# Kernel optimization log

Measured on AMD Instinct MI355X. Metric: run time of the kernel, lower is better.

## Reference

```python
import jax, jax.numpy as jnp
import numpy as np

DIM = 768   # embedding dim
NH = 12     # num heads
HD = DIM // NH  # head dim = 64
WS = 14     # window size
EPS = 1e-5  # nn.LayerNorm default


def _ln(x, w, b):
    m = jnp.mean(x, -1, keepdims=True)
    v = jnp.var(x, -1, keepdims=True)
    return (x - m) * jax.lax.rsqrt(v + EPS) * w + b


def setup_inputs() -> dict:
    key = jax.random.key(0)
    ks = jax.random.split(key, 8)
    def n(k, shape, s=0.02):
        return jax.random.normal(k, shape, jnp.float32) * s
    return {
        "x": jax.random.normal(ks[0], (4, 64, 64, DIM), jnp.float32),
        "ln1_w": jnp.ones((DIM,), jnp.float32),
        "ln1_b": jnp.zeros((DIM,), jnp.float32),
        "qkv_w": n(ks[1], (DIM, 3 * DIM)),
        "qkv_b": jnp.zeros((3 * DIM,), jnp.float32),
        "proj_w": n(ks[2], (DIM, DIM)),
        "proj_b": jnp.zeros((DIM,), jnp.float32),
        "rel_pos_h": n(ks[3], (2 * WS - 1, HD)),
        "rel_pos_w": n(ks[4], (2 * WS - 1, HD)),
        "ln2_w": jnp.ones((DIM,), jnp.float32),
        "ln2_b": jnp.zeros((DIM,), jnp.float32),
        "fc1_w": n(ks[5], (DIM, 4 * DIM)),
        "fc1_b": jnp.zeros((4 * DIM,), jnp.float32),
        "fc2_w": n(ks[6], (4 * DIM, DIM)),
        "fc2_b": jnp.zeros((DIM,), jnp.float32),
    }


def _block(x, ln1_w, ln1_b, qkv_w, qkv_b, proj_w, proj_b,
           rel_pos_h, rel_pos_w, ln2_w, ln2_b, fc1_w, fc1_b, fc2_w, fc2_b):
    B, H, W, C = x.shape
    shortcut = x
    xn = _ln(x, ln1_w, ln1_b)

    # ---- window partition (pad H,W up to multiples of WS) ----
    pad_h = (-H) % WS
    pad_w = (-W) % WS
    xp = jnp.pad(xn, ((0, 0), (0, pad_h), (0, pad_w), (0, 0)))
    Hp, Wp = H + pad_h, W + pad_w
    nh, nw = Hp // WS, Wp // WS
    xw = xp.reshape(B, nh, WS, nw, WS, C).transpose(0, 1, 3, 2, 4, 5)
    xw = xw.reshape(B * nh * nw, WS, WS, C)  # [Bw, ws, ws, C]
    Bw = B * nh * nw
    N = WS * WS

    # ---- attention with decomposed relative position bias ----
    qkv = xw.reshape(Bw, N, C) @ qkv_w + qkv_b            # [Bw, N, 3C]
    qkv = qkv.reshape(Bw, N, 3, NH, HD).transpose(2, 0, 3, 1, 4)  # [3, Bw, NH, N, HD]
    q, k, v = qkv[0], qkv[1], qkv[2]
    scale = HD ** -0.5
    attn = jnp.einsum("bhnd,bhmd->bhnm", q * scale, k)    # [Bw, NH, N, N]

    # decomposed rel pos: Rh[q_h, k_h, c], Rw[q_w, k_w, c]
    idx = jnp.arange(WS)[:, None] - jnp.arange(WS)[None, :] + (WS - 1)
    Rh = rel_pos_h[idx]  # [ws, ws, HD]
    Rw = rel_pos_w[idx]  # [ws, ws, HD]
    rq = q.reshape(Bw, NH, WS, WS, HD)
    rel_h = jnp.einsum("bnhwc,hkc->bnhwk", rq, Rh)  # over q rows vs k rows
    rel_w = jnp.einsum("bnhwc,wkc->bnhwk", rq, Rw)  # over q cols vs k cols
    attn = (attn.reshape(Bw, NH, WS, WS, WS, WS)
            + rel_h[..., :, None] + rel_w[..., None, :]).reshape(Bw, NH, N, N)

    attn = jax.nn.softmax(attn, axis=-1)
    out = jnp.einsum("bhnm,bhmd->bhnd", attn, v)          # [Bw, NH, N, HD]
    out = out.transpose(0, 2, 1, 3).reshape(Bw, WS, WS, C)
    out = out @ proj_w + proj_b

    # ---- window unpartition + crop padding ----
    out = out.reshape(B, nh, nw, WS, WS, C).transpose(0, 1, 3, 2, 4, 5)
    out = out.reshape(B, Hp, Wp, C)[:, :H, :W, :]

    x = shortcut + out

    # ---- MLP ----
    h = _ln(x, ln2_w, ln2_b)
    h = jax.nn.gelu(h @ fc1_w + fc1_b, approximate=False)
    x = x + (h @ fc2_w + fc2_b)
    return x


def reference(x, ln1_w, ln1_b, qkv_w, qkv_b, proj_w, proj_b,
              rel_pos_h, rel_pos_w, ln2_w, ln2_b, fc1_w, fc1_b, fc2_w, fc2_b):
    return _block(x, ln1_w, ln1_b, qkv_w, qkv_b, proj_w, proj_b,
                  rel_pos_h, rel_pos_w, ln2_w, ln2_b, fc1_w, fc1_b, fc2_w, fc2_b)
```

## Files before the change

### kernel.cpp

```cpp
#include <hip/hip_runtime.h>

typedef unsigned short u16;
typedef __bf16 bf16x8_t __attribute__((ext_vector_type(8)));
typedef float f32x4_t __attribute__((ext_vector_type(4)));

__device__ __forceinline__ float bf2f(u16 u) {
    union { unsigned u; float f; } c; c.u = ((unsigned)u) << 16; return c.f;
}
__device__ __forceinline__ u16 f2bf(float f) {
    union { float f; unsigned u; } c; c.f = f;
    unsigned u = c.u;
    unsigned r = (u + 0x7FFFu + ((u >> 16) & 1u)) >> 16;
    return (u16)r;
}

__device__ __forceinline__ void gld16(const u16* g, u16* l) {
    __builtin_amdgcn_global_load_lds(
        (const __attribute__((address_space(1))) unsigned*)g,
        (__attribute__((address_space(3))) unsigned*)l, 16, 0, 0);
}

__device__ __forceinline__ void block_sum2(float& s, float& sq) {
    for (int o = 32; o > 0; o >>= 1) { s += __shfl_xor(s, o); sq += __shfl_xor(sq, o); }
    __shared__ float sh[8];
    int wid = threadIdx.x >> 6;
    if ((threadIdx.x & 63) == 0) { sh[wid] = s; sh[4 + wid] = sq; }
    __syncthreads();
    s  = sh[0] + sh[1] + sh[2] + sh[3];
    sq = sh[4] + sh[5] + sh[6] + sh[7];
}

__global__ __launch_bounds__(256) void ln1_window(
    const float* __restrict__ x, const float* __restrict__ w, const float* __restrict__ b,
    u16* __restrict__ out, int row0)
{
    int lrow = blockIdx.x, tid = threadIdx.x;
    int wr = row0 + lrow;
    int wb = wr / 196, t = wr % 196;
    int gh = ((wb % 25) / 5) * 14 + t / 14;
    int gw = (wb % 5) * 14 + t % 14;
    size_t orow = (size_t)lrow * 768;
    __shared__ u16 rowbuf[768];
    if (gh >= 64 || gw >= 64) {
        rowbuf[tid] = 0; rowbuf[tid + 256] = 0; rowbuf[tid + 512] = 0;
        __syncthreads();
        if (tid < 96) *(uint4*)&out[orow + (tid << 3)] = *(const uint4*)&rowbuf[tid << 3];
        return;
    }
    size_t base = (size_t)(((wb / 25) * 64 + gh) * 64 + gw) * 768;
    float v0 = x[base + tid], v1 = x[base + tid + 256], v2 = x[base + tid + 512];
    float s = v0 + v1 + v2, sq = v0 * v0 + v1 * v1 + v2 * v2;
    block_sum2(s, sq);
    float mean = s * (1.0f / 768.0f);
    float var  = sq * (1.0f / 768.0f) - mean * mean;
    float inv  = rsqrtf(var + 1e-5f);
    rowbuf[tid]       = f2bf((v0 - mean) * inv * w[tid]       + b[tid]);
    rowbuf[tid + 256] = f2bf((v1 - mean) * inv * w[tid + 256] + b[tid + 256]);
    rowbuf[tid + 512] = f2bf((v2 - mean) * inv * w[tid + 512] + b[tid + 512]);
    __syncthreads();
    if (tid < 96) *(uint4*)&out[orow + (tid << 3)] = *(const uint4*)&rowbuf[tid << 3];
}

__global__ __launch_bounds__(256) void ln2_chunk(
    const float* __restrict__ xin, const float* __restrict__ w, const float* __restrict__ b,
    u16* __restrict__ out)
{
    int row = blockIdx.x, tid = threadIdx.x;
    size_t base = (size_t)row * 768;
    __shared__ u16 rowbuf[768];
    float v0 = xin[base + tid], v1 = xin[base + tid + 256], v2 = xin[base + tid + 512];
    float s = v0 + v1 + v2, sq = v0 * v0 + v1 * v1 + v2 * v2;
    block_sum2(s, sq);
    float mean = s * (1.0f / 768.0f);
    float var  = sq * (1.0f / 768.0f) - mean * mean;
    float inv  = rsqrtf(var + 1e-5f);
    rowbuf[tid]       = f2bf((v0 - mean) * inv * w[tid]       + b[tid]);
    rowbuf[tid + 256] = f2bf((v1 - mean) * inv * w[tid + 256] + b[tid + 256]);
    rowbuf[tid + 512] = f2bf((v2 - mean) * inv * w[tid + 512] + b[tid + 512]);
    __syncthreads();
    if (tid < 96) *(uint4*)&out[base + (tid << 3)] = *(const uint4*)&rowbuf[tid << 3];
}

__global__ __launch_bounds__(256) void transpose_wf(
    const float* __restrict__ in, u16* __restrict__ out, int K, int N)
{
    __shared__ u16 t[32][33];
    __shared__ u16 tt[32][32];
    int n0 = blockIdx.x * 32, k0 = blockIdx.y * 32;
    int tx = threadIdx.x & 31, ty = threadIdx.x >> 5;
    for (int q = 0; q < 4; q++) {
        int k = k0 + ty + q * 8, n = n0 + tx;
        t[ty + q * 8][tx] = (k < K && n < N) ? f2bf(in[(size_t)k * N + n]) : (u16)0;
    }
    __syncthreads();
    for (int q = 0; q < 4; q++) tt[ty + q * 8][tx] = t[tx][ty + q * 8];
    __syncthreads();
    if (threadIdx.x < 128) {
        int r = threadIdx.x >> 2, c8 = (threadIdx.x & 3) << 3;
        int n = n0 + r, k = k0 + c8;
        if (n < N && k < K)
            *(uint4*)&out[(size_t)n * K + k] = *(const uint4*)&tt[r][c8];
    }
}

__global__ __launch_bounds__(256) void build_relT(
    const float* __restrict__ rh, const float* __restrict__ rw, u16* __restrict__ out)
{
    int i = blockIdx.x * 256 + threadIdx.x;
    int r = i >> 6, c = i & 63;
    float v = (r < 27) ? rh[r * 64 + c] : (r < 54 ? rw[(r - 27) * 64 + c] : 0.f);
    out[i] = f2bf(v);
}

__global__ __launch_bounds__(256) void build_vt(
    const u16* __restrict__ qkvc, u16* __restrict__ vt)
{
    int z = blockIdx.x;
    int wb = z / 12, h = z % 12;
    __shared__ u16 t[64][232];
    int tid = threadIdx.x;
    for (int base = 0; base < 196; base += 4) {
        int m = base + (tid >> 6);
        int d = tid & 63;
        t[d][m] = qkvc[(size_t)(wb * 196 + m) * 2304 + 1536 + h * 64 + d];
    }
    for (int idx = tid; idx < 28 * 64; idx += 256) {
        int m = 196 + idx / 64, d = idx % 64;
        t[d][m] = 0;
    }
    __syncthreads();
    size_t ob = (size_t)z * 64 * 224;
    for (int idx = tid; idx < 64 * 28; idx += 256) {
        int d = idx / 28, c8 = (idx % 28) << 3;
        *(uint4*)&vt[ob + (size_t)d * 224 + c8] = *(const uint4*)&t[d][c8];
    }
}

__global__ __launch_bounds__(256) void softmax_rel2(
    u16* __restrict__ S, const u16* __restrict__ G2)
{
    int z = blockIdx.y;
    int wv = threadIdx.x >> 6, lane = threadIdx.x & 63;
    int n = blockIdx.x * 4 + wv;
    size_t srow = (size_t)z * 196 * 224 + (size_t)n * 224;
    const u16* g2 = G2 + (size_t)z * 196 * 64 + (size_t)n * 64;
    int qh = n / 14, qw = n % 14;
    float s[4];
    for (int c = 0; c < 4; c++) {
        int m = c * 64 + lane;
        if (m < 196) {
            int kk = m / 14, jj = m % 14;
            float bh = bf2f(g2[qh - kk + 13]);
            float bw = bf2f(g2[27 + qw - jj + 13]);
            s[c] = 0.125f * bf2f(S[srow + m]) + bh + bw;
        } else s[c] = -1e30f;
    }
    float mx = fmaxf(fmaxf(s[0], s[1]), fmaxf(s[2], s[3]));
    for (int o = 32; o > 0; o >>= 1) mx = fmaxf(mx, __shfl_xor(mx, o));
    float e[4], sm = 0.f;
    for (int c = 0; c < 4; c++) {
        int m = c * 64 + lane;
        e[c] = (m < 196) ? expf(s[c] - mx) : 0.f;
        sm += e[c];
    }
    for (int o = 32; o > 0; o >>= 1) sm += __shfl_xor(sm, o);
    float inv = 1.0f / sm;
    for (int c = 0; c < 4; c++) {
        int m = c * 64 + lane;
        if (m < 224) S[srow + m] = f2bf(e[c] * inv);
    }
}

__device__ __forceinline__ int swz_off(int row, int kcElem) {
    return row * 32 + (kcElem ^ (((row >> 1) & 3) << 3));
}

template <int MODE>
__global__ __launch_bounds__(256, 3) void gemm_nt(
    const u16* __restrict__ Aall, const u16* __restrict__ Ball,
    const float* __restrict__ bias, const float* xf,
    u16* __restrict__ Cb, float* Cf, int M, int row0)
{
    constexpr int BK = 32;
    int N, K, lda, ldb;
    size_t aoff = 0, boff = 0, coff = 0;
    if constexpr (MODE == 0) { N = 2304; K = 768; lda = 768; ldb = 768; }
    else if constexpr (MODE == 1) {
        N = 196; K = 64; lda = 2304; ldb = 2304;
        int z = blockIdx.z;
        aoff = (size_t)(z / 12) * 196 * 2304 + (size_t)(z % 12) * 64;
        boff = aoff + 768;
        coff = (size_t)z * 196 * 224;
    } else if constexpr (MODE == 2) {
        N = 64; K = 224; lda = 224; ldb = 224;
        int z = blockIdx.z;
        aoff = (size_t)z * 196 * 224;
        boff = (size_t)z * 64 * 224;
        coff = (size_t)(z / 12) * 196 * 768 + (size_t)(z % 12) * 64;
    } else if constexpr (MODE == 3) { N = 768; K = 768; lda = 768; ldb = 768; }
    else if constexpr (MODE == 4) { N = 3072; K = 768; lda = 768; ldb = 768; }
    else if constexpr (MODE == 6) {
        N = 64; K = 64; lda = 2304; ldb = 64;
        int z = blockIdx.z;
        aoff = (size_t)(z / 12) * 196 * 2304 + (size_t)(z % 12) * 64;
        boff = 0;
        coff = (size_t)z * 196 * 64;
    }
    else { N = 768; K = 3072; lda = 3072; ldb = 3072; }

    __shared__ __align__(16) u16 smem[24576];

    int tid = threadIdx.x, wid = tid >> 6, lane = tid & 63;
    int quad = lane >> 4, l16 = lane & 15;

    int bx = blockIdx.x, by = blockIdx.y;
    if constexpr (MODE != 1 && MODE != 2 && MODE != 6) {
        int gX = gridDim.x;
        int nwg = gX * gridDim.y;
        int orig = by * gX + bx;
        int q = nwg >> 3, r = nwg & 7;
        int xcd = orig & 7, idx = orig >> 3;
        int wg = (xcd < r ? xcd * (q + 1) : r * (q + 1) + (xcd - r) * q) + idx;
        bx = wg % gX; by = wg / gX;
    }
    int m_tile = by * 128, n_tile = bx * 128;
    int wm0 = (wid >> 1) * 64, wn0 = (wid & 1) * 64;

    const u16* A = Aall + aoff;
    const u16* B = Ball + boff;

    const u16* gA[2]; const u16* gB[2];
    int loff[2];
    {
        int s = lane & 3, rofs = lane >> 2;
        for (int j = 0; j < 2; j++) {
            int r0 = wid * 32 + j * 16;
            int rr = r0 + rofs;
            int xr = (rr >> 1) & 3;
            int colo = ((s ^ xr) << 3);
            int am = m_tile + rr; if (am > M - 1) am = M - 1;
            int bn = n_tile + rr; if (bn > N - 1) bn = N - 1;
            gA[j] = A + (size_t)am * lda + colo;
            gB[j] = B + (size_t)bn * ldb + colo;
            loff[j] = r0 * 32;
        }
    }

    f32x4_t acc[4][4];
    f32x4_t z4 = {0.f, 0.f, 0.f, 0.f};
    for (int mt = 0; mt < 4; mt++)
        for (int nt = 0; nt < 4; nt++) acc[mt][nt] = z4;

    int nsteps = K / BK;
    for (int j = 0; j < 2; j++) {
        gld16(gA[j], smem + loff[j]);
        gld16(gB[j], smem + 4096 + loff[j]);
    }
    for (int j = 0; j < 2; j++) {
        gld16(gA[j] + BK, smem + 8192 + loff[j]);
        gld16(gB[j] + BK, smem + 12288 + loff[j]);
    }

    int cur = 0;
    for (int k = 0; k < nsteps; k++) {
        if (k + 1 < nsteps) {
            asm volatile("s_waitcnt vmcnt(4)" ::: "memory");
        } else {
            asm volatile("s_waitcnt vmcnt(0)" ::: "memory");
        }
        __builtin_amdgcn_sched_barrier(0);
        __builtin_amdgcn_s_barrier();
        __builtin_amdgcn_sched_barrier(0);
        if (k + 2 < nsteps) {
            int nb = cur + 2; if (nb >= 3) nb -= 3;
            u16* dst = smem + nb * 8192;
            int kn = (k + 2) * BK;
            for (int j = 0; j < 2; j++) {
                gld16(gA[j] + kn, dst + loff[j]);
                gld16(gB[j] + kn, dst + 4096 + loff[j]);
            }
        }
        const u16* Ac = smem + cur * 8192;
        const u16* Bc = Ac + 4096;
        bf16x8_t af[4], bfv[4];
        for (int t = 0; t < 4; t++) {
            int ar = wm0 + t * 16 + l16;
            int br = wn0 + t * 16 + l16;
            af[t]  = *(const bf16x8_t*)&Ac[swz_off(ar, quad * 8)];
            bfv[t] = *(const bf16x8_t*)&Bc[swz_off(br, quad * 8)];
        }
        for (int mt = 0; mt < 4; mt++)
            for (int nt = 0; nt < 4; nt++)
                acc[mt][nt] = __builtin_amdgcn_mfma_f32_16x16x32_bf16(
                    af[mt], bfv[nt], acc[mt][nt], 0, 0, 0);
        cur++; if (cur >= 3) cur -= 3;
    }

    if constexpr (MODE == 0 || MODE == 1 || MODE == 2 || MODE == 4 || MODE == 6) {
        u16* Cs = smem;
        int ldc = (MODE == 0) ? 2304 : (MODE == 1) ? 224 : (MODE == 2) ? 768
                : (MODE == 6) ? 64 : 3072;
        int colmax = (MODE == 1) ? 224 : N;
        for (int half = 0; half < 2; half++) {
            __syncthreads();
            if ((wm0 >> 6) == half) {
                for (int mt = 0; mt < 4; mt++) {
                    int rl = mt * 16 + quad * 4;
                    for (int nt = 0; nt < 4; nt++) {
                        int cl = wn0 + nt * 16 + l16;
                        int col = n_tile + cl;
                        for (int rg = 0; rg < 4; rg++) {
                            float v = acc[mt][nt][rg];
                            u16 o;
                            if constexpr (MODE == 0) o = f2bf(v + bias[col]);
                            else if constexpr (MODE == 4) {
                                float g = v + bias[col];
                                o = f2bf(0.5f * g * (1.0f + erff(g * 0.70710678118f)));
                            } else o = f2bf(v);
                            Cs[(rl + rg) * 136 + cl] = o;
                        }
                    }
                }
            }
            __syncthreads();
            for (int it = 0; it < 4; it++) {
                int chunk = tid + it * 256;
                int r = chunk >> 4, c8 = (chunk & 15) << 3;
                int grow = m_tile + half * 64 + r, gcol = n_tile + c8;
                if (grow >= M || gcol >= colmax) continue;
                *(uint4*)&Cb[coff + (size_t)grow * ldc + gcol] =
                    *(const uint4*)&Cs[r * 136 + c8];
            }
        }
    } else {
        float* Cfs = (float*)smem;
        for (int q = 0; q < 4; q++) {
            __syncthreads();
            if ((wm0 >> 6) == (q >> 1)) {
                for (int mt2 = 0; mt2 < 2; mt2++) {
                    int mt = (q & 1) * 2 + mt2;
                    int rloc = mt2 * 16 + quad * 4;
                    for (int nt = 0; nt < 4; nt++) {
                        int cl = wn0 + nt * 16 + l16;
                        for (int rg = 0; rg < 4; rg++)
                            Cfs[(rloc + rg) * 132 + cl] = acc[mt][nt][rg];
                    }
                }
            }
            __syncthreads();
            for (int it = 0; it < 4; it++) {
                int chunk = tid + it * 256;
                int r = chunk >> 5, c4 = (chunk & 31) << 2;
                int grow = m_tile + q * 32 + r;
                int gcol = n_tile + c4;
                if (grow >= M || gcol >= N) continue;
                f32x4_t v4 = *(const f32x4_t*)&Cfs[r * 132 + c4];
                f32x4_t b4 = *(const f32x4_t*)&bias[gcol];
                if constexpr (MODE == 5) {
                    size_t idx = (size_t)(row0 + grow) * 768 + gcol;
                    f32x4_t x4 = *(const f32x4_t*)&xf[idx];
                    f32x4_t o4;
                    for (int j = 0; j < 4; j++) o4[j] = v4[j] + x4[j] + b4[j];
                    *(f32x4_t*)&Cf[idx] = o4;
                } else {
                    int wr = row0 + grow;
                    int wb2 = wr / 196, t2 = wr % 196;
                    int gh = ((wb2 % 25) / 5) * 14 + t2 / 14;
                    int gw = (wb2 % 5) * 14 + t2 % 14;
                    if (gh < 64 && gw < 64) {
                        size_t g = (size_t)(((wb2 / 25) * 64 + gh) * 64 + gw) * 768 + gcol;
                        f32x4_t x4 = *(const f32x4_t*)&xf[g];
                        f32x4_t o4;
                        for (int j = 0; j < 4; j++) o4[j] = v4[j] + x4[j] + b4[j];
                        *(f32x4_t*)&Cf[g] = o4;
                    }
                }
            }
        }
    }
}

extern "C" void kernel_launch(void* const* d_in, const int* in_sizes, int n_in,
                              void* d_out, int out_size, void* d_ws, size_t ws_size,
                              hipStream_t stream)
{
    (void)in_sizes; (void)n_in; (void)out_size;
    const float* x      = (const float*)d_in[0];
    const float* ln1_w  = (const float*)d_in[1];
    const float* ln1_b  = (const float*)d_in[2];
    const float* qkv_w  = (const float*)d_in[3];
    const float* qkv_b  = (const float*)d_in[4];
    const float* proj_w = (const float*)d_in[5];
    const float* proj_b = (const float*)d_in[6];
    const float* rel_h  = (const float*)d_in[7];
    const float* rel_w  = (const float*)d_in[8];
    const float* ln2_w  = (const float*)d_in[9];
    const float* ln2_b  = (const float*)d_in[10];
    const float* fc1_w  = (const float*)d_in[11];
    const float* fc1_b  = (const float*)d_in[12];
    const float* fc2_w  = (const float*)d_in[13];
    const float* fc2_b  = (const float*)d_in[14];

    const size_t WT = 14155776ull + 8192ull;
    char* ws = (char*)d_ws;
    u16* qkvT  = (u16*)ws;
    u16* projT = qkvT + 2304 * 768;
    u16* fc1T  = projT + 768 * 768;
    u16* fc2T  = fc1T + 3072 * 768;
    u16* relT  = fc2T + 3072 * 768;
    char* scratch = ws + WT;
    size_t avail = (ws_size > WT) ? (ws_size - WT) : 0;

    const size_t perW = 3204096ull;
    static const int wc_cand[8] = {100, 50, 25, 20, 10, 5, 2, 1};
    int Wc = 1;
    for (int i = 0; i < 8; i++) {
        if ((size_t)wc_cand[i] * perW <= avail) { Wc = wc_cand[i]; break; }
    }
    static const int rm_cand[8] = {16384, 8192, 4096, 2048, 1024, 512, 256, 128};
    int Rm = 128;
    for (int i = 0; i < 8; i++) {
        if ((size_t)rm_cand[i] * 7680ull <= avail) { Rm = rm_cand[i]; break; }
    }

    u16* lnwc  = (u16*)scratch;
    u16* qkvc  = (u16*)(scratch + (size_t)Wc * 301056ull);
    u16* Sc    = (u16*)(scratch + (size_t)Wc * 1204224ull);
    u16* vtc   = (u16*)(scratch + (size_t)Wc * 2257920ull);
    u16* attnc = (u16*)(scratch + (size_t)Wc * 2601984ull);
    u16* G2c   = (u16*)(scratch + (size_t)Wc * 2903040ull);
    u16* hbuf  = (u16*)scratch;
    u16* xn2c  = (u16*)(scratch + (size_t)Rm * 6144ull);
    float* dout = (float*)d_out;

    transpose_wf<<<dim3(72, 24), 256, 0, stream>>>(qkv_w, qkvT, 768, 2304);
    transpose_wf<<<dim3(24, 24), 256, 0, stream>>>(proj_w, projT, 768, 768);
    transpose_wf<<<dim3(96, 24), 256, 0, stream>>>(fc1_w, fc1T, 768, 3072);
    transpose_wf<<<dim3(24, 96), 256, 0, stream>>>(fc2_w, fc2T, 3072, 768);
    build_relT<<<16, 256, 0, stream>>>(rel_h, rel_w, relT);

    int nch = 100 / Wc;
    int rows = Wc * 196;
    int gy = (rows + 127) / 128;
    for (int c = 0; c < nch; c++) {
        int r0 = c * rows;
        ln1_window<<<rows, 256, 0, stream>>>(x, ln1_w, ln1_b, lnwc, r0);
        gemm_nt<0><<<dim3(18, gy), 256, 0, stream>>>(
            lnwc, qkvT, qkv_b, nullptr, qkvc, nullptr, rows, 0);
        gemm_nt<1><<<dim3(2, 2, Wc * 12), 256, 0, stream>>>(
            qkvc, qkvc, nullptr, nullptr, Sc, nullptr, 196, 0);
        gemm_nt<6><<<dim3(1, 2, Wc * 12), 256, 0, stream>>>(
            qkvc, relT, nullptr, nullptr, G2c, nullptr, 196, 0);
        build_vt<<<Wc * 12, 256, 0, stream>>>(qkvc, vtc);
        softmax_rel2<<<dim3(49, Wc * 12), 256, 0, stream>>>(Sc, G2c);
        gemm_nt<2><<<dim3(1, 2, Wc * 12), 256, 0, stream>>>(
            Sc, vtc, nullptr, nullptr, attnc, nullptr, 196, 0);
        gemm_nt<3><<<dim3(6, gy), 256, 0, stream>>>(
            attnc, projT, proj_b, x, nullptr, dout, rows, r0);
    }

    int nm = 16384 / Rm;
    for (int c = 0; c < nm; c++) {
        int r0 = c * Rm;
        ln2_chunk<<<Rm, 256, 0, stream>>>(dout + (size_t)r0 * 768, ln2_w, ln2_b, xn2c);
        gemm_nt<4><<<dim3(24, Rm / 128), 256, 0, stream>>>(
            xn2c, fc1T, fc1_b, nullptr, hbuf, nullptr, Rm, 0);
        gemm_nt<5><<<dim3(6, Rm / 128), 256, 0, stream>>>(
            hbuf, fc2T, fc2_b, dout, nullptr, dout, Rm, r0);
    }
}
```

Measured before the change: 753.3 us.

## Use wave-per-row layernorm, batch softmax rows, double-buffer large GEMMs

The layernorm kernels now give each 64-lane wave one row, using vector loads and shuffle-only reductions instead of an LDS staging buffer and block barrier. The softmax kernel now has each wave handle 7 rows, which cuts the grid size. The large GEMM modes switch from a 3-stage to a 2-stage LDS pipeline with a 4-block occupancy target, trading prefetch depth for more resident blocks. Attention GEMMs keep the triple-buffered path. Rows per grid must be divisible by 4, and shallower prefetch could expose memory latency.

Result: faster. 715.0 us (-5.1%).

```diff
diff --git a/kernel.cpp b/kernel.cpp
--- a/kernel.cpp
+++ b/kernel.cpp
@@ -20,65 +20,75 @@
         (__attribute__((address_space(3))) unsigned*)l, 16, 0, 0);
 }
 
-__device__ __forceinline__ void block_sum2(float& s, float& sq) {
-    for (int o = 32; o > 0; o >>= 1) { s += __shfl_xor(s, o); sq += __shfl_xor(sq, o); }
-    __shared__ float sh[8];
-    int wid = threadIdx.x >> 6;
-    if ((threadIdx.x & 63) == 0) { sh[wid] = s; sh[4 + wid] = sq; }
-    __syncthreads();
-    s  = sh[0] + sh[1] + sh[2] + sh[3];
-    sq = sh[4] + sh[5] + sh[6] + sh[7];
-}
-
 __global__ __launch_bounds__(256) void ln1_window(
     const float* __restrict__ x, const float* __restrict__ w, const float* __restrict__ b,
     u16* __restrict__ out, int row0)
 {
-    int lrow = blockIdx.x, tid = threadIdx.x;
+    int wv = threadIdx.x >> 6, lane = threadIdx.x & 63;
+    int lrow = blockIdx.x * 4 + wv;
     int wr = row0 + lrow;
     int wb = wr / 196, t = wr % 196;
     int gh = ((wb % 25) / 5) * 14 + t / 14;
     int gw = (wb % 5) * 14 + t % 14;
     size_t orow = (size_t)lrow * 768;
-    __shared__ u16 rowbuf[768];
     if (gh >= 64 || gw >= 64) {
-        rowbuf[tid] = 0; rowbuf[tid + 256] = 0; rowbuf[tid + 512] = 0;
-        __syncthreads();
-        if (tid < 96) *(uint4*)&out[orow + (tid << 3)] = *(const uint4*)&rowbuf[tid << 3];
+        uint2 zz; zz.x = 0u; zz.y = 0u;
+        for (int seg = 0; seg < 3; seg++)
+            *(uint2*)&out[orow + seg * 256 + lane * 4] = zz;
         return;
     }
     size_t base = (size_t)(((wb / 25) * 64 + gh) * 64 + gw) * 768;
-    float v0 = x[base + tid], v1 = x[base + tid + 256], v2 = x[base + tid + 512];
-    float s = v0 + v1 + v2, sq = v0 * v0 + v1 * v1 + v2 * v2;
-    block_sum2(s, sq);
+    f32x4_t v[3];
+    float s = 0.f, sq = 0.f;
+    for (int seg = 0; seg < 3; seg++) {
+        v[seg] = *(const f32x4_t*)&x[base + seg * 256 + lane * 4];
+        for (int j = 0; j < 4; j++) { s += v[seg][j]; sq += v[seg][j] * v[seg][j]; }
+    }
+    for (int o = 32; o > 0; o >>= 1) { s += __shfl_xor(s, o); sq += __shfl_xor(sq, o); }
     float mean = s * (1.0f / 768.0f);
     float var  = sq * (1.0f / 768.0f) - mean * mean;
     float inv  = rsqrtf(var + 1e-5f);
-    rowbuf[tid]       = f2bf((v0 - mean) * inv * w[tid]       + b[tid]);
-    rowbuf[tid + 256] = f2bf((v1 - mean) * inv * w[tid + 256] + b[tid + 256]);
-    rowbuf[tid + 512] = f2bf((v2 - mean) * inv * w[tid + 512] + b[tid + 512]);
-    __syncthreads();
-    if (tid < 96) *(uint4*)&out[orow + (tid << 3)] = *(const uint4*)&rowbuf[tid << 3];
+    for (int seg = 0; seg < 3; seg++) {
+        f32x4_t w4 = *(const f32x4_t*)&w[seg * 256 + lane * 4];
+        f32x4_t b4 = *(const f32x4_t*)&b[seg * 256 + lane * 4];
+        u16 o0 = f2bf((v[seg][0] - mean) * inv * w4[0] + b4[0]);
+        u16 o1 = f2bf((v[seg][1] - mean) * inv * w4[1] + b4[1]);
+        u16 o2 = f2bf((v[seg][2] - mean) * inv * w4[2] + b4[2]);
+        u16 o3 = f2bf((v[seg][3] - mean) * inv * w4[3] + b4[3]);
+        uint2 pv; pv.x = (unsigned)o0 | ((unsigned)o1 << 16);
+        pv.y = (unsigned)o2 | ((unsigned)o3 << 16);
+        *(uint2*)&out[orow + seg * 256 + lane * 4] = pv;
+    }
 }
 
 __global__ __launch_bounds__(256) void ln2_chunk(
     const float* __restrict__ xin, const float* __restrict__ w, const float* __restrict__ b,
     u16* __restrict__ out)
 {
-    int row = blockIdx.x, tid = threadIdx.x;
+    int wv = threadIdx.x >> 6, lane = threadIdx.x & 63;
+    int row = blockIdx.x * 4 + wv;
     size_t base = (size_t)row * 768;
-    __shared__ u16 rowbuf[768];
-    float v0 = xin[base + tid], v1 = xin[base + tid + 256], v2 = xin[base + tid + 512];
-    float s = v0 + v1 + v2, sq = v0 * v0 + v1 * v1 + v2 * v2;
-    block_sum2(s, sq);
+    f32x4_t v[3];
+    float s = 0.f, sq = 0.f;
+    for (int seg = 0; seg < 3; seg++) {
+        v[seg] = *(const f32x4_t*)&xin[base + seg * 256 + lane * 4];
+        for (int j = 0; j < 4; j++) { s += v[seg][j]; sq += v[seg][j] * v[seg][j]; }
+    }
+    for (int o = 32; o > 0; o >>= 1) { s += __shfl_xor(s, o); sq += __shfl_xor(sq, o); }
     float mean = s * (1.0f / 768.0f);
     float var  = sq * (1.0f / 768.0f) - mean * mean;
     float inv  = rsqrtf(var + 1e-5f);
-    rowbuf[tid]       = f2bf((v0 - mean) * inv * w[tid]       + b[tid]);
-    rowbuf[tid + 256] = f2bf((v1 - mean) * inv * w[tid + 256] + b[tid + 256]);
-    rowbuf[tid + 512] = f2bf((v2 - mean) * inv * w[tid + 512] + b[tid + 512]);
-    __syncthreads();
-    if (tid < 96) *(uint4*)&out[base + (tid << 3)] = *(const uint4*)&rowbuf[tid << 3];
+    for (int seg = 0; seg < 3; seg++) {
+        f32x4_t w4 = *(const f32x4_t*)&w[seg * 256 + lane * 4];
+        f32x4_t b4 = *(const f32x4_t*)&b[seg * 256 + lane * 4];
+        u16 o0 = f2bf((v[seg][0] - mean) * inv * w4[0] + b4[0]);
+        u16 o1 = f2bf((v[seg][1] - mean) * inv * w4[1] + b4[1]);
+        u16 o2 = f2bf((v[seg][2] - mean) * inv * w4[2] + b4[2]);
+        u16 o3 = f2bf((v[seg][3] - mean) * inv * w4[3] + b4[3]);
+        uint2 pv; pv.x = (unsigned)o0 | ((unsigned)o1 << 16);
+        pv.y = (unsigned)o2 | ((unsigned)o3 << 16);
+        *(uint2*)&out[base + seg * 256 + lane * 4] = pv;
+    }
 }
 
 __global__ __launch_bounds__(256) void transpose_wf(
@@ -141,33 +151,36 @@
 {
     int z = blockIdx.y;
     int wv = threadIdx.x >> 6, lane = threadIdx.x & 63;
-    int n = blockIdx.x * 4 + wv;
-    size_t srow = (size_t)z * 196 * 224 + (size_t)n * 224;
-    const u16* g2 = G2 + (size_t)z * 196 * 64 + (size_t)n * 64;
-    int qh = n / 14, qw = n % 14;
-    float s[4];
-    for (int c = 0; c < 4; c++) {
-        int m = c * 64 + lane;
-        if (m < 196) {
-            int kk = m / 14, jj = m % 14;
-            float bh = bf2f(g2[qh - kk + 13]);
-            float bw = bf2f(g2[27 + qw - jj + 13]);
-            s[c] = 0.125f * bf2f(S[srow + m]) + bh + bw;
-        } else s[c] = -1e30f;
-    }
-    float mx = fmaxf(fmaxf(s[0], s[1]), fmaxf(s[2], s[3]));
-    for (int o = 32; o > 0; o >>= 1) mx = fmaxf(mx, __shfl_xor(mx, o));
-    float e[4], sm = 0.f;
-    for (int c = 0; c < 4; c++) {
-        int m = c * 64 + lane;
-        e[c] = (m < 196) ? expf(s[c] - mx) : 0.f;
-        sm += e[c];
-    }
-    for (int o = 32; o > 0; o >>= 1) sm += __shfl_xor(sm, o);
-    float inv = 1.0f / sm;
-    for (int c = 0; c < 4; c++) {
-        int m = c * 64 + lane;
-        if (m < 224) S[srow + m] = f2bf(e[c] * inv);
+    int nbase = blockIdx.x * 28 + wv * 7;
+    for (int i = 0; i < 7; i++) {
+        int n = nbase + i;
+        size_t srow = (size_t)z * 196 * 224 + (size_t)n * 224;
+        const u16* g2 = G2 + (size_t)z * 196 * 64 + (size_t)n * 64;
+        int qh = n / 14, qw = n % 14;
+        float s[4];
+        for (int c = 0; c < 4; c++) {
+            int m = c * 64 + lane;
+            if (m < 196) {
+                int kk = m / 14, jj = m % 14;
+                float bh = bf2f(g2[qh - kk + 13]);
+                float bw = bf2f(g2[27 + qw - jj + 13]);
+                s[c] = 0.125f * bf2f(S[srow + m]) + bh + bw;
+            } else s[c] = -1e30f;
+        }
+        float mx = fmaxf(fmaxf(s[0], s[1]), fmaxf(s[2], s[3]));
+        for (int o = 32; o > 0; o >>= 1) mx = fmaxf(mx, __shfl_xor(mx, o));
+        float e[4], sm = 0.f;
+        for (int c = 0; c < 4; c++) {
+            int m = c * 64 + lane;
+            e[c] = (m < 196) ? expf(s[c] - mx) : 0.f;
+            sm += e[c];
+        }
+        for (int o = 32; o > 0; o >>= 1) sm += __shfl_xor(sm, o);
+        float inv = 1.0f / sm;
+        for (int c = 0; c < 4; c++) {
+            int m = c * 64 + lane;
+            if (m < 224) S[srow + m] = f2bf(e[c] * inv);
+        }
     }
 }
 
@@ -176,12 +189,14 @@
 }
 
 template <int MODE>
-__global__ __launch_bounds__(256, 3) void gemm_nt(
+__global__ __launch_bounds__(256, (MODE == 1 || MODE == 2 || MODE == 6) ? 3 : 4)
+void gemm_nt(
     const u16* __restrict__ Aall, const u16* __restrict__ Ball,
     const float* __restrict__ bias, const float* xf,
     u16* __restrict__ Cb, float* Cf, int M, int row0)
 {
     constexpr int BK = 32;
+    constexpr bool DEEP = (MODE == 1 || MODE == 2 || MODE == 6);
     int N, K, lda, ldb;
     size_t aoff = 0, boff = 0, coff = 0;
     if constexpr (MODE == 0) { N = 2304; K = 768; lda = 768; ldb = 768; }
@@ -208,7 +223,8 @@
     }
     else { N = 768; K = 3072; lda = 3072; ldb = 3072; }
 
-    __shared__ __align__(16) u16 smem[24576];
+    constexpr int NBUF = DEEP ? 3 : 2;
+    __shared__ __align__(16) u16 smem[NBUF * 8192];
 
     int tid = threadIdx.x, wid = tid >> 6, lane = tid & 63;
     int quad = lane >> 4, l16 = lane & 15;
@@ -251,49 +267,81 @@
     for (int mt = 0; mt < 4; mt++)
         for (int nt = 0; nt < 4; nt++) acc[mt][nt] = z4;
 
-    int nsteps = K / BK;
-    for (int j = 0; j < 2; j++) {
-        gld16(gA[j], smem + loff[j]);
-        gld16(gB[j], smem + 4096 + loff[j]);
-    }
-    for (int j = 0; j < 2; j++) {
-        gld16(gA[j] + BK, smem + 8192 + loff[j]);
-        gld16(gB[j] + BK, smem + 12288 + loff[j]);
-    }
-
-    int cur = 0;
-    for (int k = 0; k < nsteps; k++) {
-        if (k + 1 < nsteps) {
-            asm volatile("s_waitcnt vmcnt(4)" ::: "memory");
-        } else {
-            asm volatile("s_waitcnt vmcnt(0)" ::: "memory");
-        }
-        __builtin_amdgcn_sched_barrier(0);
-        __builtin_amdgcn_s_barrier();
-        __builtin_amdgcn_sched_barrier(0);
-        if (k + 2 < nsteps) {
-            int nb = cur + 2; if (nb >= 3) nb -= 3;
-            u16* dst = smem + nb * 8192;
-            int kn = (k + 2) * BK;
-            for (int j = 0; j < 2; j++) {
-                gld16(gA[j] + kn, dst + loff[j]);
-                gld16(gB[j] + kn, dst + 4096 + loff[j]);
-            }
-        }
-        const u16* Ac = smem + cur * 8192;
-        const u16* Bc = Ac + 4096;
-        bf16x8_t af[4], bfv[4];
-        for (int t = 0; t < 4; t++) {
-            int ar = wm0 + t * 16 + l16;
-            int br = wn0 + t * 16 + l16;
-            af[t]  = *(const bf16x8_t*)&Ac[swz_off(ar, quad * 8)];
-            bfv[t] = *(const bf16x8_t*)&Bc[swz_off(br, quad * 8)];
-        }
-        for (int mt = 0; mt < 4; mt++)
-            for (int nt = 0; nt < 4; nt++)
-                acc[mt][nt] = __builtin_amdgcn_mfma_f32_16x16x32_bf16(
-                    af[mt], bfv[nt], acc[mt][nt], 0, 0, 0);
-        cur++; if (cur >= 3) cur -= 3;
+    if constexpr (!DEEP) {
+        for (int j = 0; j < 2; j++) {
+            gld16(gA[j], smem + loff[j]);
+            gld16(gB[j], smem + 4096 + loff[j]);
+        }
+        int cur = 0;
+        for (int k0 = 0; k0 < K; k0 += BK) {
+            __syncthreads();
+            int boffc = cur << 13;
+            if (k0 + BK < K) {
+                int boffn = boffc ^ 8192;
+                for (int j = 0; j < 2; j++) {
+                    gld16(gA[j] + k0 + BK, smem + boffn + loff[j]);
+                    gld16(gB[j] + k0 + BK, smem + boffn + 4096 + loff[j]);
+                }
+            }
+            const u16* Ac = smem + boffc;
+            const u16* Bc = smem + boffc + 4096;
+            bf16x8_t af[4], bfv[4];
+            for (int t = 0; t < 4; t++) {
+                int ar = wm0 + t * 16 + l16;
+                int br = wn0 + t * 16 + l16;
+                af[t]  = *(const bf16x8_t*)&Ac[swz_off(ar, quad * 8)];
+                bfv[t] = *(const bf16x8_t*)&Bc[swz_off(br, quad * 8)];
+            }
+            for (int mt = 0; mt < 4; mt++)
+                for (int nt = 0; nt < 4; nt++)
+                    acc[mt][nt] = __builtin_amdgcn_mfma_f32_16x16x32_bf16(
+                        af[mt], bfv[nt], acc[mt][nt], 0, 0, 0);
+            cur ^= 1;
+        }
+    } else {
+        int nsteps = K / BK;
+        for (int j = 0; j < 2; j++) {
+            gld16(gA[j], smem + loff[j]);
+            gld16(gB[j], smem + 4096 + loff[j]);
+        }
+        for (int j = 0; j < 2; j++) {
+            gld16(gA[j] + BK, smem + 8192 + loff[j]);
+            gld16(gB[j] + BK, smem + 12288 + loff[j]);
+        }
+        int cur = 0;
+        for (int k = 0; k < nsteps; k++) {
+            if (k + 1 < nsteps) {
+                asm volatile("s_waitcnt vmcnt(4)" ::: "memory");
+            } else {
+                asm volatile("s_waitcnt vmcnt(0)" ::: "memory");
+            }
+            __builtin_amdgcn_sched_barrier(0);
+            __builtin_amdgcn_s_barrier();
+            __builtin_amdgcn_sched_barrier(0);
+            if (k + 2 < nsteps) {
+                int nb = cur + 2; if (nb >= 3) nb -= 3;
+                u16* dst = smem + nb * 8192;
+                int kn = (k + 2) * BK;
+                for (int j = 0; j < 2; j++) {
+                    gld16(gA[j] + kn, dst + loff[j]);
+                    gld16(gB[j] + kn, dst + 4096 + loff[j]);
+                }
+            }
+            const u16* Ac = smem + cur * 8192;
+            const u16* Bc = Ac + 4096;
+            bf16x8_t af[4], bfv[4];
+            for (int t = 0; t < 4; t++) {
+                int ar = wm0 + t * 16 + l16;
+                int br = wn0 + t * 16 + l16;
+                af[t]  = *(const bf16x8_t*)&Ac[swz_off(ar, quad * 8)];
+                bfv[t] = *(const bf16x8_t*)&Bc[swz_off(br, quad * 8)];
+            }
+            for (int mt = 0; mt < 4; mt++)
+                for (int nt = 0; nt < 4; nt++)
+                    acc[mt][nt] = __builtin_amdgcn_mfma_f32_16x16x32_bf16(
+                        af[mt], bfv[nt], acc[mt][nt], 0, 0, 0);
+            cur++; if (cur >= 3) cur -= 3;
+        }
     }
 
     if constexpr (MODE == 0 || MODE == 1 || MODE == 2 || MODE == 4 || MODE == 6) {
@@ -444,7 +492,7 @@
     int gy = (rows + 127) / 128;
     for (int c = 0; c < nch; c++) {
         int r0 = c * rows;
-        ln1_window<<<rows, 256, 0, stream>>>(x, ln1_w, ln1_b, lnwc, r0);
+        ln1_window<<<rows / 4, 256, 0, stream>>>(x, ln1_w, ln1_b, lnwc, r0);
         gemm_nt<0><<<dim3(18, gy), 256, 0, stream>>>(
             lnwc, qkvT, qkv_b, nullptr, qkvc, nullptr, rows, 0);
         gemm_nt<1><<<dim3(2, 2, Wc * 12), 256, 0, stream>>>(
@@ -452,7 +500,7 @@
         gemm_nt<6><<<dim3(1, 2, Wc * 12), 256, 0, stream>>>(
             qkvc, relT, nullptr, nullptr, G2c, nullptr, 196, 0);
         build_vt<<<Wc * 12, 256, 0, stream>>>(qkvc, vtc);
-        softmax_rel2<<<dim3(49, Wc * 12), 256, 0, stream>>>(Sc, G2c);
+        softmax_rel2<<<dim3(7, Wc * 12), 256, 0, stream>>>(Sc, G2c);
         gemm_nt<2><<<dim3(1, 2, Wc * 12), 256, 0, stream>>>(
             Sc, vtc, nullptr, nullptr, attnc, nullptr, 196, 0);
         gemm_nt<3><<<dim3(6, gy), 256, 0, stream>>>(
@@ -462,7 +510,7 @@
     int nm = 16384 / Rm;
     for (int c = 0; c < nm; c++) {
         int r0 = c * Rm;
-        ln2_chunk<<<Rm, 256, 0, stream>>>(dout + (size_t)r0 * 768, ln2_w, ln2_b, xn2c);
+        ln2_chunk<<<Rm / 4, 256, 0, stream>>>(dout + (size_t)r0 * 768, ln2_w, ln2_b, xn2c);
         gemm_nt<4><<<dim3(24, Rm / 128), 256, 0, stream>>>(
             xn2c, fc1T, fc1_b, nullptr, hbuf, nullptr, Rm, 0);
         gemm_nt<5><<<dim3(6, Rm / 128), 256, 0, stream>>>(
```
